# Kernel optimization log

Measured on AMD Instinct MI355X. Metric: run time of the kernel, lower is better.

## Reference

```python
import jax, jax.numpy as jnp
import numpy as np

B, N_HEADS, DIM, HS, WS = 8, 8, 256, 64, 64
CH = DIM // N_HEADS          # 32 head dim
HIDDEN = max(DIM // 2, 32)   # 128 SE hidden (r=2)
SCALE = CH ** -0.5
# CoaT-style CRPE: window sizes 3,5,7 over head groups (2,3,3)

def _dwconv(x, w, b):
    # depthwise conv, x: [B, Cg, H, W], w: [Cg, 1, kw, kw]
    y = jax.lax.conv_general_dilated(
        x, w, (1, 1), 'SAME',
        dimension_numbers=('NCHW', 'OIHW', 'NCHW'),
        feature_group_count=x.shape[1])
    return y + b[None, :, None, None]

def setup_inputs() -> dict:
    key = jax.random.key(0)
    ks = jax.random.split(key, 8)
    s = 0.02
    return {
        'x': jax.random.normal(ks[0], (B, HS * WS, DIM), jnp.float32),
        'qkv_w': jax.random.normal(ks[1], (3 * DIM, DIM), jnp.float32) * s,
        'qkv_b': jnp.zeros((3 * DIM,), jnp.float32),
        'proj_w': jax.random.normal(ks[2], (DIM, DIM), jnp.float32) * s,
        'proj_b': jnp.zeros((DIM,), jnp.float32),
        'se_w1': jax.random.normal(ks[3], (HIDDEN, DIM), jnp.float32) * s,
        'se_w2': jax.random.normal(ks[4], (N_HEADS, HIDDEN), jnp.float32) * s,
        'crpe_w3': jax.random.normal(ks[5], (2 * CH, 1, 3, 3), jnp.float32) * s,
        'crpe_b3': jnp.zeros((2 * CH,), jnp.float32),
        'crpe_w5': jax.random.normal(ks[6], (3 * CH, 1, 5, 5), jnp.float32) * s,
        'crpe_b5': jnp.zeros((3 * CH,), jnp.float32),
        'crpe_w7': jax.random.normal(ks[7], (3 * CH, 1, 7, 7), jnp.float32) * s,
        'crpe_b7': jnp.zeros((3 * CH,), jnp.float32),
        'H': HS, 'W': WS,
    }

def _crpe(q, v, H, W, w3, b3, w5, b5, w7, b7):
    # q, v: [B, h, N, Ch]; N == H*W
    Bq, h, N, Ch = q.shape
    v_img = v.transpose(0, 1, 3, 2).reshape(Bq, h * Ch, H, W)
    c0, c1 = 2 * Ch, 5 * Ch  # head splits (2,3,3)
    y = jnp.concatenate([
        _dwconv(v_img[:, :c0], w3, b3),
        _dwconv(v_img[:, c0:c1], w5, b5),
        _dwconv(v_img[:, c1:], w7, b7),
    ], axis=1)
    conv_v = y.reshape(Bq, h, Ch, N).transpose(0, 1, 3, 2)
    return q * conv_v  # Hadamard rel-pos term

def reference(x, qkv_w, qkv_b, proj_w, proj_b, se_w1, se_w2,
              crpe_w3, crpe_b3, crpe_w5, crpe_b5, crpe_w7, crpe_b7, H, W):
    Bx, N, C = x.shape
    qkv = (x @ qkv_w.T + qkv_b).reshape(Bx, N, 3, N_HEADS, CH)
    qkv = qkv.transpose(2, 0, 3, 1, 4)  # [3, B, h, N, Ch]
    q, k, v = qkv[0], qkv[1], qkv[2]
    crpe = _crpe(q, v, H, W, crpe_w3, crpe_b3, crpe_w5, crpe_b5, crpe_w7, crpe_b7)
    k_softmax = jax.nn.softmax(k, axis=2)  # softmax over tokens N
    ktv = jnp.einsum('bhnk,bhnv->bhkv', k_softmax, v)     # [B,h,Ch,Ch]
    factor_att = jnp.einsum('bhnk,bhkv->bhnv', q, ktv)    # [B,h,N,Ch]
    factor_att = SCALE * factor_att + crpe
    # SE-style domain gating: mean-pool over N -> conv1x1 -> relu -> conv1x1 -> sigmoid
    pooled = factor_att.mean(axis=2).reshape(Bx, N_HEADS * CH)  # [B, C]
    hid = jax.nn.relu(pooled @ se_w1.T)                         # [B, HIDDEN]
    gate = jax.nn.sigmoid(hid @ se_w2.T)                        # [B, h]
    out = factor_att * (1.0 + gate[:, :, None, None])           # gate*fa + fa
    out = out.transpose(0, 2, 1, 3).reshape(Bx, N, C)
    return out @ proj_w.T + proj_b
```

## Files before the change

kernel.cpp:

```cpp
#include <hip/hip_runtime.h>

namespace {

constexpr float kScale = 0.17677669529663687f;

typedef __attribute__((ext_vector_type(8))) short bf16x8;
typedef __attribute__((ext_vector_type(4))) short bf16x4;
typedef __attribute__((ext_vector_type(4))) float f32x4;

__device__ __forceinline__ short bf_hi(float x) {
  unsigned u = __float_as_uint(x);
  return (short)((u + 0x7FFFu + ((u >> 16) & 1u)) >> 16);
}
__device__ __forceinline__ short bf_lo(float x) {
  unsigned u = __float_as_uint(x);
  unsigned hi = (u + 0x7FFFu + ((u >> 16) & 1u)) & 0xFFFF0000u;
  float r = x - __uint_as_float(hi);
  unsigned u2 = __float_as_uint(r);
  return (short)((u2 + 0x7FFFu + ((u2 >> 16) & 1u)) >> 16);
}

__global__ __launch_bounds__(1024) void wsplit2_kernel(
    const float* __restrict__ w, short* __restrict__ wsplit2) {
  const int nc = blockIdx.x;
  const int ct = nc / 24, j = nc % 24;
  const int r = j >> 3, kc = j & 7;
  const bool lo = (r == 1);
  const int u = threadIdx.x;
  const int col = u >> 2, kq = u & 3;
  const float* src = &w[(size_t)(ct * 256 + col) * 256 + kc * 32 + kq * 8];
  const float4 f0 = *reinterpret_cast<const float4*>(src);
  const float4 f1 = *reinterpret_cast<const float4*>(src + 4);
  bf16x8 v;
  if (lo) {
    v[0] = bf_lo(f0.x); v[1] = bf_lo(f0.y); v[2] = bf_lo(f0.z);
    v[3] = bf_lo(f0.w); v[4] = bf_lo(f1.x); v[5] = bf_lo(f1.y);
    v[6] = bf_lo(f1.z); v[7] = bf_lo(f1.w);
  } else {
    v[0] = bf_hi(f0.x); v[1] = bf_hi(f0.y); v[2] = bf_hi(f0.z);
    v[3] = bf_hi(f0.w); v[4] = bf_hi(f1.x); v[5] = bf_hi(f1.y);
    v[6] = bf_hi(f1.z); v[7] = bf_hi(f1.w);
  }
  *reinterpret_cast<bf16x8*>(&wsplit2[(size_t)nc * 8192 + u * 8]) = v;
}

__global__ __launch_bounds__(512, 1) void qkv_mfma_kernel(
    const float* __restrict__ x, const short* __restrict__ wsplit2,
    const float* __restrict__ bias, float* __restrict__ q,
    float* __restrict__ kk, float* __restrict__ v) {
  __shared__ short As[128][520];
  __shared__ short Bs[256][40];
  const int tid = threadIdx.x;
  const int row0 = blockIdx.x * 128;
  const int wave = tid >> 6, lane = tid & 63;
  const int wr = (wave >> 2) * 64;
  const int wc = (wave & 3) * 64;
  const int l15 = lane & 15, l4 = lane >> 4;
  const int bcol = tid >> 2, bkq = tid & 3;

  bf16x8 brgA[2], brgB[2];
  auto bload = [&](int nc, bf16x8 (&brg)[2]) {
    const short* src = wsplit2 + (size_t)nc * 8192;
#pragma unroll
    for (int i = 0; i < 2; ++i)
      brg[i] = *reinterpret_cast<const bf16x8*>(src + (tid + i * 512) * 8);
  };
  bload(0, brgA);
  bload(1, brgB);

#pragma unroll 4
  for (int i = 0; i < 16; ++i) {
    const int f = tid + i * 512;
    const int r = f >> 6, c = (f & 63) * 4;
    const float4 a4 = *reinterpret_cast<const float4*>(
        &x[(size_t)(row0 + r) * 256 + c]);
    bf16x4 h, l;
    h[0] = bf_hi(a4.x); h[1] = bf_hi(a4.y); h[2] = bf_hi(a4.z);
    h[3] = bf_hi(a4.w);
    l[0] = bf_lo(a4.x); l[1] = bf_lo(a4.y); l[2] = bf_lo(a4.z);
    l[3] = bf_lo(a4.w);
    *reinterpret_cast<bf16x4*>(&As[r][c]) = h;
    *reinterpret_cast<bf16x4*>(&As[r][256 + c]) = l;
  }
  __syncthreads();

  f32x4 acc[4][4];
  auto step = [&](int nc, bf16x8 (&brg)[2]) {
#pragma unroll
    for (int i = 0; i < 2; ++i) {
      const int u = tid + i * 512;
      *reinterpret_cast<bf16x8*>(&Bs[u >> 2][(u & 3) * 8]) = brg[i];
    }
    __syncthreads();
    if (nc + 2 < 72) bload(nc + 2, brg);
    const int j = nc % 24;
    const int r = j >> 3, kc = j & 7;
    const int aoff = (r == 2 ? 256 : 0) + kc * 32;
    bf16x8 af[4], bfr[4];
#pragma unroll
    for (int f = 0; f < 4; ++f) {
      af[f] = *reinterpret_cast<const bf16x8*>(
          &As[wr + f * 16 + l15][aoff + l4 * 8]);
      bfr[f] = *reinterpret_cast<const bf16x8*>(&Bs[wc + f * 16 + l15][l4 * 8]);
    }
#pragma unroll
    for (int fi = 0; fi < 4; ++fi)
#pragma unroll
      for (int fj = 0; fj < 4; ++fj)
        acc[fi][fj] = __builtin_amdgcn_mfma_f32_16x16x32_bf16(
            af[fi], bfr[fj], acc[fi][fj], 0, 0, 0);
    __syncthreads();
  };

  for (int ct = 0; ct < 3; ++ct) {
#pragma unroll
    for (int i = 0; i < 4; ++i)
#pragma unroll
      for (int j = 0; j < 4; ++j) acc[i][j] = (f32x4){0.f, 0.f, 0.f, 0.f};

    for (int j2 = 0; j2 < 12; ++j2) {
      step(ct * 24 + j2 * 2, brgA);
      step(ct * 24 + j2 * 2 + 1, brgB);
    }
    float* dst = (ct == 0) ? q : (ct == 1) ? kk : v;
#pragma unroll
    for (int fj = 0; fj < 4; ++fj) {
      const int col = wc + fj * 16 + l15;
      const int hh = col >> 5, cc = col & 31;
      const float bv = bias[ct * 256 + col];
#pragma unroll
      for (int fi = 0; fi < 4; ++fi) {
#pragma unroll
        for (int jj = 0; jj < 4; ++jj) {
          const int rr = row0 + wr + fi * 16 + l4 * 4 + jj;
          const int bb = rr >> 12, n = rr & 4095;
          dst[((size_t)(bb * 8 + hh) * 4096 + n) * 32 + cc] =
              acc[fi][fj][jj] + bv;
        }
      }
    }
  }
}

__global__ __launch_bounds__(256) void ktv_partial_kernel(
    const float* __restrict__ k, const float* __restrict__ v,
    float* __restrict__ pev, float* __restrict__ pe) {
  const int bh = blockIdx.x;
  const int chunk = blockIdx.y;
  const float* kb = k + (size_t)bh * 131072 + (size_t)chunk * 256 * 32;
  const float* vb = v + (size_t)bh * 131072 + (size_t)chunk * 256 * 32;
  __shared__ __align__(16) float ks[32][32];
  __shared__ __align__(16) float vs[32][32];
  const int t = threadIdx.x;
  const int kc = t >> 3;
  const int vg = (t & 7) * 4;
  const int sr = t >> 3, sc = (t & 7) * 4;
  float a0 = 0.f, a1 = 0.f, a2 = 0.f, a3 = 0.f, se = 0.f;
  for (int n0 = 0; n0 < 256; n0 += 32) {
    __syncthreads();
    const float4 k4 =
        *reinterpret_cast<const float4*>(&kb[(size_t)(n0 + sr) * 32 + sc]);
    const float4 v4 =
        *reinterpret_cast<const float4*>(&vb[(size_t)(n0 + sr) * 32 + sc]);
    *reinterpret_cast<float4*>(&ks[sr][sc]) = k4;
    *reinterpret_cast<float4*>(&vs[sr][sc]) = v4;
    __syncthreads();
#pragma unroll
    for (int r = 0; r < 32; ++r) {
      const float e = __expf(ks[r][kc]);
      se += e;
      const float4 vv = *reinterpret_cast<const float4*>(&vs[r][vg]);
      a0 = fmaf(e, vv.x, a0); a1 = fmaf(e, vv.y, a1);
      a2 = fmaf(e, vv.z, a2); a3 = fmaf(e, vv.w, a3);
    }
  }
  float* o = pev + ((size_t)(bh * 16 + chunk)) * 1024 + kc * 32 + vg;
  o[0] = a0; o[1] = a1; o[2] = a2; o[3] = a3;
  if ((t & 7) == 0) pe[(bh * 16 + chunk) * 32 + kc] = se;
}

__global__ __launch_bounds__(256) void ktv_reduce_kernel(
    const float* __restrict__ pev, const float* __restrict__ pe,
    float* __restrict__ ktv) {
  const int bh = blockIdx.x;
  const int t = threadIdx.x;
  const int kc = t >> 3, vg = (t & 7) * 4;
  float a0 = 0.f, a1 = 0.f, a2 = 0.f, a3 = 0.f, se = 0.f;
  for (int ch = 0; ch < 16; ++ch) {
    const float4 p4 = *reinterpret_cast<const float4*>(
        &pev[((size_t)(bh * 16 + ch)) * 1024 + kc * 32 + vg]);
    a0 += p4.x; a1 += p4.y; a2 += p4.z; a3 += p4.w;
    se += pe[(bh * 16 + ch) * 32 + kc];
  }
  const float inv = 1.0f / se;
  float* o = ktv + (size_t)bh * 1024 + kc * 32 + vg;
  o[0] = a0 * inv; o[1] = a1 * inv; o[2] = a2 * inv; o[3] = a3 * inv;
}

template <int K>
__device__ __forceinline__ void crpe_tile(const float (*lds)[64][32],
                                          const float* __restrict__ wch,
                                          float bias, int c, int x0,
                                          float* __restrict__ outbase) {
  constexpr int P = K / 2;
  constexpr int W = 8 + K - 1;
  float wreg[K * K];
#pragma unroll
  for (int i = 0; i < K * K; ++i) wreg[i] = wch[i];
#pragma unroll
  for (int yy = 0; yy < 4; ++yy) {
    float acc[8];
#pragma unroll
    for (int i = 0; i < 8; ++i) acc[i] = bias;
#pragma unroll
    for (int ky = 0; ky < K; ++ky) {
      const int lrow = yy + ky + (3 - P);
      float win[W];
#pragma unroll
      for (int j = 0; j < W; ++j) {
        const int xx = x0 + j - P;
        const int xc = min(max(xx, 0), 63);
        const float val = lds[lrow][xc][c];
        win[j] = (xx == xc) ? val : 0.f;
      }
#pragma unroll
      for (int kx = 0; kx < K; ++kx) {
        const float wgt = wreg[ky * K + kx];
#pragma unroll
        for (int i = 0; i < 8; ++i) acc[i] = fmaf(win[i + kx], wgt, acc[i]);
      }
    }
#pragma unroll
    for (int i = 0; i < 8; ++i)
      outbase[(size_t)(yy * 64 + x0 + i) * 32 + c] = acc[i];
  }
}

__global__ __launch_bounds__(256) void crpe_conv_kernel(
    const float* __restrict__ v, const float* __restrict__ w3,
    const float* __restrict__ b3, const float* __restrict__ w5,
    const float* __restrict__ b5, const float* __restrict__ w7,
    const float* __restrict__ b7, float* __restrict__ convv) {
  __shared__ __align__(16) float lds[10][64][32];
  const int t = threadIdx.x;
  const int y0 = blockIdx.x * 4;
  const int h = blockIdx.y, b = blockIdx.z;
  const float* vb = v + (size_t)(b * 8 + h) * 131072;
  const int ytop = y0 - 3;
  float4* lds4 = reinterpret_cast<float4*>(&lds[0][0][0]);
#pragma unroll
  for (int i = 0; i < 20; ++i) {
    const int idx = t + i * 256;
    const int row = idx >> 9;
    const int y = ytop + row;
    float4 val = {0.f, 0.f, 0.f, 0.f};
    if (y >= 0 && y < 64)
      val = *reinterpret_cast<const float4*>(
          &vb[(size_t)y * 2048 + (size_t)(idx & 511) * 4]);
    lds4[idx] = val;
  }
  __syncthreads();
  const int c = t & 31;
  const int x0 = (t >> 5) * 8;
  const int ch = h * 32 + c;
  float* outbase = convv + ((size_t)(b * 8 + h) * 4096 + y0 * 64) * 32;
  if (h < 2)
    crpe_tile<3>(lds, w3 + ch * 9, b3[ch], c, x0, outbase);
  else if (h < 5)
    crpe_tile<5>(lds, w5 + (ch - 64) * 25, b5[ch - 64], c, x0, outbase);
  else
    crpe_tile<7>(lds, w7 + (ch - 160) * 49, b7[ch - 160], c, x0, outbase);
}

__global__ __launch_bounds__(256) void factor_att_kernel(
    const float* __restrict__ q, const float* __restrict__ convv,
    const float* __restrict__ ktv, float* __restrict__ fa,
    float* __restrict__ partial) {
  const int b = blockIdx.z, h = blockIdx.y;
  const int n0 = blockIdx.x * 64;
  __shared__ __align__(16) float kt[32][32];
  __shared__ float qs[8][32];
  __shared__ float ps[8][32];
  const int t = threadIdx.x;
#pragma unroll
  for (int i = 0; i < 4; ++i) {
    const int idx = t + i * 256;
    kt[idx >> 5][idx & 31] = ktv[(size_t)(b * 8 + h) * 1024 + idx];
  }
  const size_t off = ((size_t)(b * 8 + h) * 4096 + n0) * 32;
  const float* qb = q + off;
  const float* cb = convv + off;
  float* fb = fa + off;
  const int c = t & 31, rs = t >> 5;
  float pool = 0.f;
  for (int i = 0; i < 8; ++i) {
    __syncthreads();
    qs[rs][c] = qb[i * 256 + t];
    __syncthreads();
    float s = 0.f;
#pragma unroll
    for (int kc = 0; kc < 32; ++kc) s = fmaf(qs[rs][kc], kt[kc][c], s);
    const float val = kScale * s + qs[rs][c] * cb[i * 256 + t];
    fb[i * 256 + t] = val;
    pool += val;
  }
  __syncthreads();
  ps[rs][c] = pool;
  __syncthreads();
  if (t < 32) {
    float s = 0.f;
#pragma unroll
    for (int r = 0; r < 8; ++r) s += ps[r][t];
    partial[((size_t)(b * 8 + h) * 64 + blockIdx.x) * 32 + t] = s;
  }
}

__global__ __launch_bounds__(256) void se_kernel(
    const float* __restrict__ partial, const float* __restrict__ w1,
    const float* __restrict__ w2, float* __restrict__ gfac) {
  const int b = blockIdx.x, t = threadIdx.x;
  __shared__ float pm[256];
  __shared__ float hid[128];
  {
    const int h = t >> 5, c = t & 31;
    const float* p = partial + ((size_t)(b * 8 + h) * 64) * 32 + c;
    float s = 0.f;
#pragma unroll 8
    for (int nc = 0; nc < 64; ++nc) s += p[nc * 32];
    pm[t] = s * (1.0f / 4096.0f);
  }
  __syncthreads();
  if (t < 128) {
    float s = 0.f;
    for (int ch = 0; ch < 256; ++ch) s = fmaf(pm[ch], w1[t * 256 + ch], s);
    hid[t] = fmaxf(s, 0.f);
  }
  __syncthreads();
  if (t < 8) {
    float g = 0.f;
    for (int j = 0; j < 128; ++j) g = fmaf(hid[j], w2[t * 128 + j], g);
    gfac[b * 8 + t] = 1.0f + 1.0f / (1.0f + __expf(-g));
  }
}

__global__ __launch_bounds__(256, 2) void proj_mfma_kernel(
    const float* __restrict__ fa, const float* __restrict__ gfac,
    const float* __restrict__ w, const float* __restrict__ bias,
    float* __restrict__ out) {
  __shared__ short As[128][72];
  __shared__ short Bs[128][72];
  const int tid = threadIdx.x;
  const int row0 = blockIdx.y * 128;
  const int col0 = blockIdx.x * 128;
  const int wave = tid >> 6, lane = tid & 63;
  const int wr = (wave >> 1) * 64, wc = (wave & 1) * 64;
  const int l15 = lane & 15, l4 = lane >> 4;
  const int srow = tid >> 3, schunk = tid & 7;
  const int b = row0 >> 12;
  f32x4 acc[4][4];
#pragma unroll
  for (int i = 0; i < 4; ++i)
#pragma unroll
    for (int j = 0; j < 4; ++j) acc[i][j] = (f32x4){0.f, 0.f, 0.f, 0.f};

  for (int k0 = 0; k0 < 768; k0 += 64) {
    const int ksrc = k0 & 255;
    const bool alo = (k0 >= 512);
    const bool blo = (k0 >= 256) && (k0 < 512);
    __syncthreads();
#pragma unroll
    for (int i = 0; i < 4; ++i) {
      const int r = srow + i * 32;
      const int ch = ksrc + schunk * 8;
      const int hh = ch >> 5, cc = ch & 31;
      const int n = (row0 & 4095) + r;
      const float g = gfac[b * 8 + hh];
      const float* sa = &fa[((size_t)(b * 8 + hh) * 4096 + n) * 32 + cc];
      float4 a0 = *reinterpret_cast<const float4*>(sa);
      float4 a1 = *reinterpret_cast<const float4*>(sa + 4);
      a0.x *= g; a0.y *= g; a0.z *= g; a0.w *= g;
      a1.x *= g; a1.y *= g; a1.z *= g; a1.w *= g;
      bf16x8 va, vb;
      if (alo) {
        va[0] = bf_lo(a0.x); va[1] = bf_lo(a0.y); va[2] = bf_lo(a0.z);
        va[3] = bf_lo(a0.w); va[4] = bf_lo(a1.x); va[5] = bf_lo(a1.y);
        va[6] = bf_lo(a1.z); va[7] = bf_lo(a1.w);
      } else {
        va[0] = bf_hi(a0.x); va[1] = bf_hi(a0.y); va[2] = bf_hi(a0.z);
        va[3] = bf_hi(a0.w); va[4] = bf_hi(a1.x); va[5] = bf_hi(a1.y);
        va[6] = bf_hi(a1.z); va[7] = bf_hi(a1.w);
      }
      *reinterpret_cast<bf16x8*>(&As[r][schunk * 8]) = va;
      const float* sb = &w[(size_t)(col0 + r) * 256 + ch];
      const float4 b0 = *reinterpret_cast<const float4*>(sb);
      const float4 b1 = *reinterpret_cast<const float4*>(sb + 4);
      if (blo) {
        vb[0] = bf_lo(b0.x); vb[1] = bf_lo(b0.y); vb[2] = bf_lo(b0.z);
        vb[3] = bf_lo(b0.w); vb[4] = bf_lo(b1.x); vb[5] = bf_lo(b1.y);
        vb[6] = bf_lo(b1.z); vb[7] = bf_lo(b1.w);
      } else {
        vb[0] = bf_hi(b0.x); vb[1] = bf_hi(b0.y); vb[2] = bf_hi(b0.z);
        vb[3] = bf_hi(b0.w); vb[4] = bf_hi(b1.x); vb[5] = bf_hi(b1.y);
        vb[6] = bf_hi(b1.z); vb[7] = bf_hi(b1.w);
      }
      *reinterpret_cast<bf16x8*>(&Bs[r][schunk * 8]) = vb;
    }
    __syncthreads();
#pragma unroll
    for (int ks = 0; ks < 2; ++ks) {
      bf16x8 af[4], bfr[4];
#pragma unroll
      for (int f = 0; f < 4; ++f) {
        af[f] = *reinterpret_cast<const bf16x8*>(
            &As[wr + f * 16 + l15][ks * 32 + l4 * 8]);
        bfr[f] = *reinterpret_cast<const bf16x8*>(
            &Bs[wc + f * 16 + l15][ks * 32 + l4 * 8]);
      }
#pragma unroll
      for (int fi = 0; fi < 4; ++fi)
#pragma unroll
        for (int fj = 0; fj < 4; ++fj)
          acc[fi][fj] = __builtin_amdgcn_mfma_f32_16x16x32_bf16(
              af[fi], bfr[fj], acc[fi][fj], 0, 0, 0);
    }
  }
#pragma unroll
  for (int fj = 0; fj < 4; ++fj) {
    const int col = col0 + wc + fj * 16 + l15;
    const float bv = bias[col];
#pragma unroll
    for (int fi = 0; fi < 4; ++fi) {
#pragma unroll
      for (int j = 0; j < 4; ++j) {
        const int r = row0 + wr + fi * 16 + l4 * 4 + j;
        out[(size_t)r * 256 + col] = acc[fi][fj][j] + bv;
      }
    }
  }
}

}

extern "C" void kernel_launch(void* const* d_in, const int* in_sizes, int n_in,
                              void* d_out, int out_size, void* d_ws,
                              size_t ws_size, hipStream_t stream) {
  const float* x      = (const float*)d_in[0];
  const float* qkv_w  = (const float*)d_in[1];
  const float* qkv_b  = (const float*)d_in[2];
  const float* proj_w = (const float*)d_in[3];
  const float* proj_b = (const float*)d_in[4];
  const float* se_w1  = (const float*)d_in[5];
  const float* se_w2  = (const float*)d_in[6];
  const float* w3 = (const float*)d_in[7];
  const float* b3 = (const float*)d_in[8];
  const float* w5 = (const float*)d_in[9];
  const float* b5 = (const float*)d_in[10];
  const float* w7 = (const float*)d_in[11];
  const float* b7 = (const float*)d_in[12];
  float* out = (float*)d_out;
  float* ws = (float*)d_ws;

  const size_t SZ = (size_t)8 * 8 * 4096 * 32;
  float* q       = ws;
  float* kbuf    = ws + SZ;
  float* vbuf    = ws + 2 * SZ;
  float* ktv     = ws + 3 * SZ;
  float* kmaxp   = ktv + 65536;
  float* partial = kmaxp + 16384;
  float* gfac    = partial + 131072;
  float* pev = out;
  float* pe  = out + 64 * 16 * 1024;
  short* wsplit2 = (short*)(out + 2 * 1024 * 1024);
  (void)ws_size; (void)in_sizes; (void)n_in; (void)out_size;

  wsplit2_kernel<<<72, 1024, 0, stream>>>(qkv_w, wsplit2);
  qkv_mfma_kernel<<<256, 512, 0, stream>>>(x, wsplit2, qkv_b, q, kbuf, vbuf);
  ktv_partial_kernel<<<dim3(64, 16), 256, 0, stream>>>(kbuf, vbuf, pev, pe);
  ktv_reduce_kernel<<<64, 256, 0, stream>>>(pev, pe, ktv);
  crpe_conv_kernel<<<dim3(16, 8, 8), 256, 0, stream>>>(vbuf, w3, b3, w5, b5,
                                                       w7, b7, kbuf);
  factor_att_kernel<<<dim3(64, 8, 8), 256, 0, stream>>>(q, kbuf, ktv, vbuf,
                                                        partial);
  se_kernel<<<8, 256, 0, stream>>>(partial, se_w1, se_w2, gfac);
  proj_mfma_kernel<<<dim3(2, 256), 256, 0, stream>>>(vbuf, gfac, proj_w,
                                                     proj_b, out);
}
```

Baseline: 216.5 us.

## Restructure proj GEMM to full-width tiles with pre-split bf16 weights

Each proj block now covers 128 rows by all 256 output columns. Its activation tile is converted once into hi/lo bf16 halves held in shared memory. The weight matrix is pre-split into hi/lo bf16 by a new kernel and streamed from a double-buffered register prefetch, mirroring the qkv kernel. This removes the duplicated activation loading and float-to-bf16 conversion across the two column blocks, and the per-iteration weight conversion. The cost is one extra small kernel launch, less occupancy (512 threads, one block per CU, large LDS) and reuse of the q buffer as scratch.

```diff
diff --git a/kernel.cpp b/kernel.cpp
--- a/kernel.cpp
+++ b/kernel.cpp
@@ -18,6 +18,21 @@
   float r = x - __uint_as_float(hi);
   unsigned u2 = __float_as_uint(r);
   return (short)((u2 + 0x7FFFu + ((u2 >> 16) & 1u)) >> 16);
+}
+
+__device__ __forceinline__ bf16x8 cvt8v(const float4 f0, const float4 f1,
+                                        bool lo) {
+  bf16x8 v;
+  if (lo) {
+    v[0] = bf_lo(f0.x); v[1] = bf_lo(f0.y); v[2] = bf_lo(f0.z);
+    v[3] = bf_lo(f0.w); v[4] = bf_lo(f1.x); v[5] = bf_lo(f1.y);
+    v[6] = bf_lo(f1.z); v[7] = bf_lo(f1.w);
+  } else {
+    v[0] = bf_hi(f0.x); v[1] = bf_hi(f0.y); v[2] = bf_hi(f0.z);
+    v[3] = bf_hi(f0.w); v[4] = bf_hi(f1.x); v[5] = bf_hi(f1.y);
+    v[6] = bf_hi(f1.z); v[7] = bf_hi(f1.w);
+  }
+  return v;
 }
 
 __global__ __launch_bounds__(1024) void wsplit2_kernel(
@@ -31,17 +46,22 @@
   const float* src = &w[(size_t)(ct * 256 + col) * 256 + kc * 32 + kq * 8];
   const float4 f0 = *reinterpret_cast<const float4*>(src);
   const float4 f1 = *reinterpret_cast<const float4*>(src + 4);
-  bf16x8 v;
-  if (lo) {
-    v[0] = bf_lo(f0.x); v[1] = bf_lo(f0.y); v[2] = bf_lo(f0.z);
-    v[3] = bf_lo(f0.w); v[4] = bf_lo(f1.x); v[5] = bf_lo(f1.y);
-    v[6] = bf_lo(f1.z); v[7] = bf_lo(f1.w);
-  } else {
-    v[0] = bf_hi(f0.x); v[1] = bf_hi(f0.y); v[2] = bf_hi(f0.z);
-    v[3] = bf_hi(f0.w); v[4] = bf_hi(f1.x); v[5] = bf_hi(f1.y);
-    v[6] = bf_hi(f1.z); v[7] = bf_hi(f1.w);
-  }
-  *reinterpret_cast<bf16x8*>(&wsplit2[(size_t)nc * 8192 + u * 8]) = v;
+  *reinterpret_cast<bf16x8*>(&wsplit2[(size_t)nc * 8192 + u * 8]) =
+      cvt8v(f0, f1, lo);
+}
+
+__global__ __launch_bounds__(1024) void pwsplit_kernel(
+    const float* __restrict__ w, short* __restrict__ pw) {
+  const int nc = blockIdx.x;
+  const int r = nc >> 3, kc = nc & 7;
+  const bool lo = (r == 1);
+  const int u = threadIdx.x;
+  const int col = u >> 2, kq = u & 3;
+  const float* src = &w[(size_t)col * 256 + kc * 32 + kq * 8];
+  const float4 f0 = *reinterpret_cast<const float4*>(src);
+  const float4 f1 = *reinterpret_cast<const float4*>(src + 4);
+  *reinterpret_cast<bf16x8*>(&pw[(size_t)nc * 8192 + u * 8]) =
+      cvt8v(f0, f1, lo);
 }
 
 __global__ __launch_bounds__(512, 1) void qkv_mfma_kernel(
@@ -56,7 +76,6 @@
   const int wr = (wave >> 2) * 64;
   const int wc = (wave & 3) * 64;
   const int l15 = lane & 15, l4 = lane >> 4;
-  const int bcol = tid >> 2, bkq = tid & 3;
 
   bf16x8 brgA[2], brgB[2];
   auto bload = [&](int nc, bf16x8 (&brg)[2]) {
@@ -343,97 +362,96 @@
   }
 }
 
-__global__ __launch_bounds__(256, 2) void proj_mfma_kernel(
+__global__ __launch_bounds__(512, 1) void proj_mfma_kernel(
     const float* __restrict__ fa, const float* __restrict__ gfac,
-    const float* __restrict__ w, const float* __restrict__ bias,
+    const short* __restrict__ pwsplit, const float* __restrict__ bias,
     float* __restrict__ out) {
-  __shared__ short As[128][72];
-  __shared__ short Bs[128][72];
+  __shared__ short As[128][520];
+  __shared__ short Bs[256][40];
   const int tid = threadIdx.x;
-  const int row0 = blockIdx.y * 128;
-  const int col0 = blockIdx.x * 128;
+  const int row0 = blockIdx.x * 128;
   const int wave = tid >> 6, lane = tid & 63;
-  const int wr = (wave >> 1) * 64, wc = (wave & 1) * 64;
+  const int wr = (wave >> 2) * 64;
+  const int wc = (wave & 3) * 64;
   const int l15 = lane & 15, l4 = lane >> 4;
-  const int srow = tid >> 3, schunk = tid & 7;
   const int b = row0 >> 12;
+
+  bf16x8 brgA[2], brgB[2];
+  auto bload = [&](int nc, bf16x8 (&brg)[2]) {
+    const short* src = pwsplit + (size_t)nc * 8192;
+#pragma unroll
+    for (int i = 0; i < 2; ++i)
+      brg[i] = *reinterpret_cast<const bf16x8*>(src + (tid + i * 512) * 8);
+  };
+  bload(0, brgA);
+  bload(1, brgB);
+
+#pragma unroll 4
+  for (int i = 0; i < 16; ++i) {
+    const int f = tid + i * 512;
+    const int r = f >> 6, c = (f & 63) * 4;
+    const int hh = c >> 5, cc = c & 31;
+    const int n = (row0 & 4095) + r;
+    const float g = gfac[b * 8 + hh];
+    float4 a4 = *reinterpret_cast<const float4*>(
+        &fa[((size_t)(b * 8 + hh) * 4096 + n) * 32 + cc]);
+    a4.x *= g; a4.y *= g; a4.z *= g; a4.w *= g;
+    bf16x4 h, l;
+    h[0] = bf_hi(a4.x); h[1] = bf_hi(a4.y); h[2] = bf_hi(a4.z);
+    h[3] = bf_hi(a4.w);
+    l[0] = bf_lo(a4.x); l[1] = bf_lo(a4.y); l[2] = bf_lo(a4.z);
+    l[3] = bf_lo(a4.w);
+    *reinterpret_cast<bf16x4*>(&As[r][c]) = h;
+    *reinterpret_cast<bf16x4*>(&As[r][256 + c]) = l;
+  }
+  __syncthreads();
+
   f32x4 acc[4][4];
 #pragma unroll
   for (int i = 0; i < 4; ++i)
 #pragma unroll
     for (int j = 0; j < 4; ++j) acc[i][j] = (f32x4){0.f, 0.f, 0.f, 0.f};
 
-  for (int k0 = 0; k0 < 768; k0 += 64) {
-    const int ksrc = k0 & 255;
-    const bool alo = (k0 >= 512);
-    const bool blo = (k0 >= 256) && (k0 < 512);
-    __syncthreads();
-#pragma unroll
-    for (int i = 0; i < 4; ++i) {
-      const int r = srow + i * 32;
-      const int ch = ksrc + schunk * 8;
-      const int hh = ch >> 5, cc = ch & 31;
-      const int n = (row0 & 4095) + r;
-      const float g = gfac[b * 8 + hh];
-      const float* sa = &fa[((size_t)(b * 8 + hh) * 4096 + n) * 32 + cc];
-      float4 a0 = *reinterpret_cast<const float4*>(sa);
-      float4 a1 = *reinterpret_cast<const float4*>(sa + 4);
-      a0.x *= g; a0.y *= g; a0.z *= g; a0.w *= g;
-      a1.x *= g; a1.y *= g; a1.z *= g; a1.w *= g;
-      bf16x8 va, vb;
-      if (alo) {
-        va[0] = bf_lo(a0.x); va[1] = bf_lo(a0.y); va[2] = bf_lo(a0.z);
-        va[3] = bf_lo(a0.w); va[4] = bf_lo(a1.x); va[5] = bf_lo(a1.y);
-        va[6] = bf_lo(a1.z); va[7] = bf_lo(a1.w);
-      } else {
-        va[0] = bf_hi(a0.x); va[1] = bf_hi(a0.y); va[2] = bf_hi(a0.z);
-        va[3] = bf_hi(a0.w); va[4] = bf_hi(a1.x); va[5] = bf_hi(a1.y);
-        va[6] = bf_hi(a1.z); va[7] = bf_hi(a1.w);
-      }
-      *reinterpret_cast<bf16x8*>(&As[r][schunk * 8]) = va;
-      const float* sb = &w[(size_t)(col0 + r) * 256 + ch];
-      const float4 b0 = *reinterpret_cast<const float4*>(sb);
-      const float4 b1 = *reinterpret_cast<const float4*>(sb + 4);
-      if (blo) {
-        vb[0] = bf_lo(b0.x); vb[1] = bf_lo(b0.y); vb[2] = bf_lo(b0.z);
-        vb[3] = bf_lo(b0.w); vb[4] = bf_lo(b1.x); vb[5] = bf_lo(b1.y);
-        vb[6] = bf_lo(b1.z); vb[7] = bf_lo(b1.w);
-      } else {
-        vb[0] = bf_hi(b0.x); vb[1] = bf_hi(b0.y); vb[2] = bf_hi(b0.z);
-        vb[3] = bf_hi(b0.w); vb[4] = bf_hi(b1.x); vb[5] = bf_hi(b1.y);
-        vb[6] = bf_hi(b1.z); vb[7] = bf_hi(b1.w);
-      }
-      *reinterpret_cast<bf16x8*>(&Bs[r][schunk * 8]) = vb;
-    }
-    __syncthreads();
-#pragma unroll
-    for (int ks = 0; ks < 2; ++ks) {
-      bf16x8 af[4], bfr[4];
-#pragma unroll
-      for (int f = 0; f < 4; ++f) {
-        af[f] = *reinterpret_cast<const bf16x8*>(
-            &As[wr + f * 16 + l15][ks * 32 + l4 * 8]);
-        bfr[f] = *reinterpret_cast<const bf16x8*>(
-            &Bs[wc + f * 16 + l15][ks * 32 + l4 * 8]);
-      }
-#pragma unroll
-      for (int fi = 0; fi < 4; ++fi)
-#pragma unroll
-        for (int fj = 0; fj < 4; ++fj)
-          acc[fi][fj] = __builtin_amdgcn_mfma_f32_16x16x32_bf16(
-              af[fi], bfr[fj], acc[fi][fj], 0, 0, 0);
-    }
+  auto step = [&](int nc, bf16x8 (&brg)[2]) {
+#pragma unroll
+    for (int i = 0; i < 2; ++i) {
+      const int u = tid + i * 512;
+      *reinterpret_cast<bf16x8*>(&Bs[u >> 2][(u & 3) * 8]) = brg[i];
+    }
+    __syncthreads();
+    if (nc + 2 < 24) bload(nc + 2, brg);
+    const int r = nc >> 3, kc = nc & 7;
+    const int aoff = (r == 2 ? 256 : 0) + kc * 32;
+    bf16x8 af[4], bfr[4];
+#pragma unroll
+    for (int f = 0; f < 4; ++f) {
+      af[f] = *reinterpret_cast<const bf16x8*>(
+          &As[wr + f * 16 + l15][aoff + l4 * 8]);
+      bfr[f] = *reinterpret_cast<const bf16x8*>(&Bs[wc + f * 16 + l15][l4 * 8]);
+    }
+#pragma unroll
+    for (int fi = 0; fi < 4; ++fi)
+#pragma unroll
+      for (int fj = 0; fj < 4; ++fj)
+        acc[fi][fj] = __builtin_amdgcn_mfma_f32_16x16x32_bf16(
+            af[fi], bfr[fj], acc[fi][fj], 0, 0, 0);
+    __syncthreads();
+  };
+
+  for (int j2 = 0; j2 < 12; ++j2) {
+    step(j2 * 2, brgA);
+    step(j2 * 2 + 1, brgB);
   }
 #pragma unroll
   for (int fj = 0; fj < 4; ++fj) {
-    const int col = col0 + wc + fj * 16 + l15;
+    const int col = wc + fj * 16 + l15;
     const float bv = bias[col];
 #pragma unroll
     for (int fi = 0; fi < 4; ++fi) {
 #pragma unroll
-      for (int j = 0; j < 4; ++j) {
-        const int r = row0 + wr + fi * 16 + l4 * 4 + j;
-        out[(size_t)r * 256 + col] = acc[fi][fj][j] + bv;
+      for (int jj = 0; jj < 4; ++jj) {
+        const int rr = row0 + wr + fi * 16 + l4 * 4 + jj;
+        out[(size_t)rr * 256 + col] = acc[fi][fj][jj] + bv;
       }
     }
   }
@@ -471,6 +489,7 @@
   float* pev = out;
   float* pe  = out + 64 * 16 * 1024;
   short* wsplit2 = (short*)(out + 2 * 1024 * 1024);
+  short* pwsplit = (short*)q;
   (void)ws_size; (void)in_sizes; (void)n_in; (void)out_size;
 
   wsplit2_kernel<<<72, 1024, 0, stream>>>(qkv_w, wsplit2);
@@ -482,6 +501,6 @@
   factor_att_kernel<<<dim3(64, 8, 8), 256, 0, stream>>>(q, kbuf, ktv, vbuf,
                                                         partial);
   se_kernel<<<8, 256, 0, stream>>>(partial, se_w1, se_w2, gfac);
-  proj_mfma_kernel<<<dim3(2, 256), 256, 0, stream>>>(vbuf, gfac, proj_w,
-                                                     proj_b, out);
-}
+  pwsplit_kernel<<<24, 1024, 0, stream>>>(proj_w, pwsplit);
+  proj_mfma_kernel<<<256, 512, 0, stream>>>(vbuf, gfac, pwsplit, proj_b, out);
+}
```

Measured after the change: 180.5 us. -16.6%, faster.
